# Kernel optimization log

Measured on AMD Instinct MI355X. Metric: run time of the kernel, lower is better.

## Reference

```python
import jax, jax.numpy as jnp
import numpy as np
from jax import lax

B, CH, TS = 64, 9, 3000
D, H, EMB = 64, 256, 32
WIDTHS = (3, 2, 2, 2, 2, 2)
IN_CH = (1, H, H, H, H, H)
OUT_CH = (H, H, H, H, H, D)


def setup_inputs():
    keys = iter(jax.random.split(jax.random.key(0), 64))
    inp = {"x": jax.random.normal(next(keys), (B, CH, TS), jnp.float32)}
    for l, (ci, co, w) in enumerate(zip(IN_CH, OUT_CH, WIDTHS)):
        inp[f"conv_w{l}"] = jax.random.normal(next(keys), (co, ci, w), jnp.float32) / np.float32(np.sqrt(ci * w))
        inp[f"conv_b{l}"] = jnp.zeros((co,), jnp.float32)
        inp[f"gn_g{l}"] = jnp.ones((co,), jnp.float32)
        inp[f"gn_b{l}"] = jnp.zeros((co,), jnp.float32)
    inp["ro_w"] = jax.random.normal(next(keys), (D, D), jnp.float32) / np.float32(np.sqrt(D))
    inp["ro_b"] = jnp.zeros((D,), jnp.float32)
    for r in range(2):
        inp[f"msg_w{r}"] = jax.random.normal(next(keys), (2 * D, D), jnp.float32) / np.float32(np.sqrt(2 * D))
        inp[f"msg_b{r}"] = jnp.zeros((D,), jnp.float32)
    inp["rn_w1"] = jax.random.normal(next(keys), (D, D), jnp.float32) / np.float32(np.sqrt(D))
    inp["rn_b1"] = jnp.zeros((D,), jnp.float32)
    inp["rn_w2"] = jax.random.normal(next(keys), (D, D), jnp.float32) / np.float32(np.sqrt(D))
    inp["rn_b2"] = jnp.zeros((D,), jnp.float32)
    inp["proj_w"] = jax.random.normal(next(keys), (D, EMB), jnp.float32) / np.float32(np.sqrt(D))
    inp["proj_b"] = jnp.zeros((EMB,), jnp.float32)
    return inp


def _gn(h, g, b):
    # GroupNorm(num_groups=1): normalize over (C, T) per sample
    mu = h.mean(axis=(1, 2), keepdims=True)
    var = h.var(axis=(1, 2), keepdims=True)
    return (h - mu) * lax.rsqrt(var + 1e-5) * g[None, :, None] + b[None, :, None]


def _forward(x, ps):
    b, ch, ts = x.shape
    h = x.reshape(b * ch, 1, ts)  # each view is one 1-channel node signal
    for l, w in enumerate(WIDTHS):
        W, bi, g, be = ps[4 * l], ps[4 * l + 1], ps[4 * l + 2], ps[4 * l + 3]
        h = lax.conv_general_dilated(h, W, (w,), [(w // 2, w // 2)], dimension_numbers=("NCH", "OIH", "NCH")) + bi[None, :, None]
        h = jax.nn.gelu(_gn(h, g, be), approximate=False)
    ro_w, ro_b = ps[24], ps[25]
    h = jnp.einsum("nct,co->not", h, ro_w) + ro_b[None, :, None]  # 1x1 readout conv
    lat = h.transpose(0, 2, 1)  # [b*ch, T, D]
    N = b * ch
    # fully-connected graph within each sample, exactly as in the torch code
    msg_from = np.repeat(np.arange(N), ch - 1)
    grid = np.broadcast_to(np.arange(N).reshape(b, ch)[:, None, :], (b, ch, ch))
    msg_to = grid[:, ~np.eye(ch, dtype=bool)].reshape(-1)
    for W, bi in ((ps[26], ps[27]), (ps[28], ps[29])):
        m = jnp.concatenate([lat[msg_from], lat[msg_to]], axis=-1)  # [E, T, 2D]
        m = jax.nn.relu(m @ W + bi) / (ch - 1)  # dropout is identity at eval
        lat = lat.at[msg_to].add(m)
    view_id = np.repeat(np.arange(b), ch)
    y = jax.ops.segment_sum(lat, view_id, num_segments=b)  # [b, T, D]
    y = (jax.nn.relu(y @ ps[30] + ps[31]) @ ps[32] + ps[33]) / ch
    return (y @ ps[34] + ps[35]).transpose(0, 2, 1)  # [b, EMB, T]


def reference(x, conv_w0, conv_b0, gn_g0, gn_b0, conv_w1, conv_b1, gn_g1, gn_b1, conv_w2, conv_b2, gn_g2, gn_b2, conv_w3, conv_b3, gn_g3, gn_b3, conv_w4, conv_b4, gn_g4, gn_b4, conv_w5, conv_b5, gn_g5, gn_b5, ro_w, ro_b, msg_w0, msg_b0, msg_w1, msg_b1, rn_w1, rn_b1, rn_w2, rn_b2, proj_w, proj_b):
    ps = (conv_w0, conv_b0, gn_g0, gn_b0, conv_w1, conv_b1, gn_g1, gn_b1, conv_w2, conv_b2, gn_g2, gn_b2, conv_w3, conv_b3, gn_g3, gn_b3, conv_w4, conv_b4, gn_g4, gn_b4, conv_w5, conv_b5, gn_g5, gn_b5, ro_w, ro_b, msg_w0, msg_b0, msg_w1, msg_b1, rn_w1, rn_b1, rn_w2, rn_b2, proj_w, proj_b)
    return _forward(x, ps)
```

## Files before the change

kernel.cpp:

```cpp
#include <hip/hip_runtime.h>
#include <hip/hip_bf16.h>

typedef __hip_bfloat16 bf16;
typedef __attribute__((ext_vector_type(8))) short s8v;
typedef __attribute__((ext_vector_type(4))) float f4v;

__device__ __forceinline__ float gelu_f(float x) {
    float x2 = x * x;
    float z  = x * __builtin_fmaf(0.071355f, x2, 1.595769f);
    float e  = __expf(-z);
    return x * __builtin_amdgcn_rcpf(1.0f + e);
}
__device__ __forceinline__ unsigned short f2bf_u(float f) {
    bf16 b = __float2bfloat16(f);
    return *(unsigned short*)&b;
}
__device__ __forceinline__ float bfu2f(unsigned short u) {
    bf16 b = *(bf16*)&u;
    return __bfloat162float(b);
}

__global__ __launch_bounds__(256) void zero_k(float* __restrict__ p, int n) {
    int i = blockIdx.x * 256 + threadIdx.x;
    if (i < n) p[i] = 0.f;
}

__global__ __launch_bounds__(256) void wcvt_k(
    const float* __restrict__ w1, const float* __restrict__ w2,
    const float* __restrict__ w3, const float* __restrict__ w4,
    const float* __restrict__ w5, bf16* __restrict__ dst)
{
    int i = blockIdx.x * 256 + threadIdx.x;
    if (i >= 557056) return;
    const float* src; int li;
    if      (i < 131072) { src = w1; li = i; }
    else if (i < 262144) { src = w2; li = i - 131072; }
    else if (i < 393216) { src = w3; li = i - 262144; }
    else if (i < 524288) { src = w4; li = i - 393216; }
    else                 { src = w5; li = i - 524288; }
    int co = li >> 9, rem = li & 511;
    int kc = rem >> 6, rr = rem & 63;
    int s = rr >> 5, cil = rr & 31;
    dst[i] = __float2bfloat16(src[co * 512 + (kc * 32 + cil) * 2 + s]);
}

__global__ __launch_bounds__(256) void m0red_k(
    const float* __restrict__ W0, const float* __restrict__ b0,
    float* __restrict__ coef, float* __restrict__ w0t)
{
    __shared__ float red[256];
    const int co = threadIdx.x;
    float w0 = W0[3 * co], w1 = W0[3 * co + 1], w2 = W0[3 * co + 2], b = b0[co];
    w0t[co] = w0; w0t[256 + co] = w1; w0t[512 + co] = w2;
    float vals[14] = {w0, w1, w2, b,
                      w0 * w0, w1 * w1, w2 * w2, b * b,
                      2.f * w0 * w1, 2.f * w0 * w2, 2.f * w1 * w2,
                      2.f * w0 * b, 2.f * w1 * b, 2.f * w2 * b};
    for (int k = 0; k < 14; k++) {
        red[co] = vals[k];
        __syncthreads();
        for (int st = 128; st > 0; st >>= 1) {
            if (co < st) red[co] += red[co + st];
            __syncthreads();
        }
        if (co == 0) coef[k] = red[0];
        __syncthreads();
    }
}

__global__ __launch_bounds__(256) void c0stats_k(
    const float* __restrict__ x, const float* __restrict__ coef,
    float* __restrict__ mu0, float* __restrict__ rstd0)
{
    __shared__ float xsl[3008];
    __shared__ float red[512];
    const int n = blockIdx.x, tid = threadIdx.x;
    const float* xr = x + (size_t)n * 3000;
    for (int i = tid; i < 750; i += 256) *(float4*)&xsl[4 + 4 * i] = *(const float4*)(xr + 4 * i);
    if (tid < 4) xsl[tid] = 0.f;
    float c[14];
    #pragma unroll
    for (int k = 0; k < 14; k++) c[k] = coef[k];
    __syncthreads();
    float S = 0.f, Q = 0.f;
    if (tid < 250) {
        float f[16];
        #pragma unroll
        for (int k = 0; k < 4; k++) *(float4*)&f[4 * k] = *(const float4*)&xsl[12 * tid + 4 * k];
        #pragma unroll
        for (int j = 0; j < 4; j++) {
            float x0 = f[3 * j + 3], x1 = f[3 * j + 4], x2 = f[3 * j + 5];
            S += c[0] * x0 + c[1] * x1 + c[2] * x2 + c[3];
            Q += c[4] * x0 * x0 + c[5] * x1 * x1 + c[6] * x2 * x2 + c[7]
               + c[8] * x0 * x1 + c[9] * x0 * x2 + c[10] * x1 * x2
               + c[11] * x0 + c[12] * x1 + c[13] * x2;
        }
    }
    red[tid] = S; red[256 + tid] = Q;
    __syncthreads();
    for (int st = 128; st > 0; st >>= 1) {
        if (tid < st) { red[tid] += red[tid + st]; red[256 + tid] += red[256 + tid + st]; }
        __syncthreads();
    }
    if (tid == 0) {
        float m = red[0] * (1.f / 256000.f);
        float var = red[256] * (1.f / 256000.f) - m * m;
        mu0[n] = m;
        rstd0[n] = rsqrtf(var + 1e-5f);
    }
}

template<int MW, int NW, int MODE>
__global__ __launch_bounds__(256) void convT_k(
    const bf16* __restrict__ g, const float* __restrict__ xraw,
    const float* __restrict__ w0t, const bf16* __restrict__ Wp,
    const float* __restrict__ bias, const float* __restrict__ b0c,
    bf16* __restrict__ hout, float* __restrict__ ssum, float* __restrict__ ssq,
    int T_g, int T_out, int n0,
    const float* __restrict__ pssum, const float* __restrict__ pssq,
    const float* __restrict__ pgam, const float* __restrict__ pbet,
    float pinvCT)
{
    constexpr int CO = 4 * NW * 16;
    constexpr int MT = MW * 16;
    constexpr int NSLOT = MT * 8;
    constexpr int NU = (NSLOT + 255) / 256;
    __shared__ bf16 aT[MT * 64];
    __shared__ float biasS[CO];
    __shared__ float red[512];
    __shared__ float acoS[256], ccoS[256];
    __shared__ float xs[(MODE == 2) ? 400 : 1];
    __shared__ float w0s[(MODE == 2) ? 768 : 1];
    const int n  = blockIdx.y;
    const int t0 = blockIdx.x * MT;
    const int tid = threadIdx.x;
    for (int i = tid; i < CO; i += 256) biasS[i] = bias[i];
    if (MODE == 1) {
        float mu = pssum[n0 + n] * pinvCT;
        float rs = rsqrtf(pssq[n0 + n] * pinvCT - mu * mu + 1e-5f);
        float a = rs * pgam[tid];
        acoS[tid] = a;
        ccoS[tid] = pbet[tid] - mu * a;
        __syncthreads();
    } else {
        float mu = pssum[n];
        float rs = pssq[n];
        float a = rs * pgam[tid];
        acoS[tid] = a;
        ccoS[tid] = (b0c[tid] - mu) * a + pbet[tid];
        for (int i = tid; i < 768; i += 256) w0s[i] = w0t[i];
        const float* xr = xraw + (size_t)n * 3000;
        for (int i = tid; i < 400; i += 256) {
            int xg = 6 * t0 - 4 + i;
            xs[i] = ((unsigned)xg < 3000u) ? xr[xg] : 0.f;
        }
        __syncthreads();
    }
    const int w = tid >> 6, lane = tid & 63;
    const int l16 = lane & 15, quad = lane >> 4;
    const int sx = l16 & 7;
    const bf16* gb = (MODE == 2) ? nullptr : (g + (size_t)n * T_g * 256);

    bool s_inv[NU];
    int s_q[NU], s_tin[NU], s_off[NU];
    #pragma unroll
    for (int u = 0; u < NU; u++) {
        int slot = tid + 256 * u;
        s_inv[u] = (NSLOT % 256 != 0) && (slot >= NSLOT);
        if (s_inv[u]) { s_tin[u] = 0x7fffffff; s_q[u] = 0; s_off[u] = 0; continue; }
        int t = slot >> 3, j = slot & 7;
        int ks = j >> 2, q = j & 3;
        s_q[u] = q;
        s_tin[u] = 2 * (t0 + t) - 1 + ks;
        s_off[u] = (t * 8 + (j ^ (t & 7))) * 8;
    }

    f4v acc[MW][NW];
    #pragma unroll
    for (int i = 0; i < MW; i++)
        #pragma unroll
        for (int j = 0; j < NW; j++) acc[i][j] = (f4v){0.f, 0.f, 0.f, 0.f};

    for (int kc = 0; kc < 8; kc++) {
        #pragma unroll
        for (int u = 0; u < NU; u++) {
            if (s_inv[u]) continue;
            int tin = s_tin[u];
            s8v v = (s8v){0, 0, 0, 0, 0, 0, 0, 0};
            if ((unsigned)tin < (unsigned)T_g) {
                const int ci0 = kc * 32 + s_q[u] * 8;
                float4 a0 = *(const float4*)&acoS[ci0], a1 = *(const float4*)&acoS[ci0 + 4];
                float4 c0 = *(const float4*)&ccoS[ci0], c1 = *(const float4*)&ccoS[ci0 + 4];
                float av[8] = {a0.x, a0.y, a0.z, a0.w, a1.x, a1.y, a1.z, a1.w};
                float cv[8] = {c0.x, c0.y, c0.z, c0.w, c1.x, c1.y, c1.z, c1.w};
                unsigned short* uu = (unsigned short*)&v;
                if (MODE == 2) {
                    int lx = 3 * (tin - 2 * t0) + 3;
                    float x0 = xs[lx], x1 = xs[lx + 1], x2 = xs[lx + 2];
                    float4 wa0 = *(const float4*)&w0s[ci0],       wa1 = *(const float4*)&w0s[ci0 + 4];
                    float4 wb0 = *(const float4*)&w0s[256 + ci0], wb1 = *(const float4*)&w0s[256 + ci0 + 4];
                    float4 wc0 = *(const float4*)&w0s[512 + ci0], wc1 = *(const float4*)&w0s[512 + ci0 + 4];
                    float wav[8] = {wa0.x, wa0.y, wa0.z, wa0.w, wa1.x, wa1.y, wa1.z, wa1.w};
                    float wbv[8] = {wb0.x, wb0.y, wb0.z, wb0.w, wb1.x, wb1.y, wb1.z, wb1.w};
                    float wcv[8] = {wc0.x, wc0.y, wc0.z, wc0.w, wc1.x, wc1.y, wc1.z, wc1.w};
                    #pragma unroll
                    for (int jj = 0; jj < 8; jj++) {
                        float conv = wav[jj] * x0 + wbv[jj] * x1 + wcv[jj] * x2;
                        uu[jj] = f2bf_u(gelu_f(conv * av[jj] + cv[jj]));
                    }
                } else {
                    v = *(const s8v*)(gb + (size_t)tin * 256 + ci0);
                    #pragma unroll
                    for (int jj = 0; jj < 8; jj++)
                        uu[jj] = f2bf_u(gelu_f(bfu2f(uu[jj]) * av[jj] + cv[jj]));
                }
            }
            *(s8v*)&aT[s_off[u]] = v;
        }
        s8v bfr[2][NW];
        #pragma unroll
        for (int ks = 0; ks < 2; ks++)
            #pragma unroll
            for (int j = 0; j < NW; j++) {
                int co = w * NW * 16 + j * 16 + l16;
                bfr[ks][j] = *(const s8v*)(Wp + (size_t)co * 512 + kc * 64 + ks * 32 + quad * 8);
            }
        __syncthreads();
        __builtin_amdgcn_s_setprio(1);
        #pragma unroll
        for (int ks = 0; ks < 2; ks++) {
            const int sl = (ks * 4 + quad) ^ sx;
            s8v af[MW];
            #pragma unroll
            for (int i = 0; i < MW; i++)
                af[i] = *(const s8v*)&aT[(i * 16 + l16) * 64 + sl * 8];
            #pragma unroll
            for (int i = 0; i < MW; i++)
                #pragma unroll
                for (int j = 0; j < NW; j++)
                    acc[i][j] = __builtin_amdgcn_mfma_f32_16x16x32_bf16(af[i], bfr[ks][j], acc[i][j], 0, 0, 0);
        }
        __builtin_amdgcn_s_setprio(0);
        __syncthreads();
    }

    float lsum = 0.f, lsq = 0.f;
    #pragma unroll
    for (int i = 0; i < MW; i++) {
        #pragma unroll
        for (int r = 0; r < 4; r++) {
            int t = t0 + i * 16 + quad * 4 + r;
            if (t < T_out) {
                bf16* orow = hout + ((size_t)n * T_out + t) * CO;
                #pragma unroll
                for (int j = 0; j < NW; j++) {
                    int co = w * NW * 16 + j * 16 + l16;
                    float v = acc[i][j][r] + biasS[co];
                    orow[co] = __float2bfloat16(v);
                    lsum += v; lsq += v * v;
                }
            }
        }
    }
    red[tid] = lsum; red[256 + tid] = lsq;
    __syncthreads();
    for (int st = 128; st > 0; st >>= 1) {
        if (tid < st) { red[tid] += red[tid + st]; red[256 + tid] += red[256 + tid + st]; }
        __syncthreads();
    }
    if (tid == 0) { atomicAdd(&ssum[n0 + n], red[0]); atomicAdd(&ssq[n0 + n], red[256]); }
}

__global__ __launch_bounds__(256) void readout_pre_k(
    const bf16* __restrict__ h5T, const float* __restrict__ row,
    const float* __restrict__ rob, const float* __restrict__ g5,
    const float* __restrict__ be5, const float* __restrict__ ssum,
    const float* __restrict__ ssq, float invCT,
    const float* __restrict__ mw, const float* __restrict__ mb,
    float* __restrict__ lat0, float* __restrict__ A0, float* __restrict__ Bv0)
{
    __shared__ float lh[2112];
    __shared__ float ll[2112];
    __shared__ float lw[8192];
    __shared__ float lb[64];
    const int n = blockIdx.x, tid = threadIdx.x;
    const float mu = ssum[n] * invCT;
    const float rs = rsqrtf(ssq[n] * invCT - mu * mu + 1e-5f);
    for (int idx = tid; idx < 2112; idx += 256) {
        int c = idx & 63;
        float a = rs * g5[c];
        float v = __bfloat162float(h5T[(size_t)n * 2112 + idx]) * a + (be5[c] - mu * a);
        lh[idx] = gelu_f(v);
    }
    for (int idx = tid; idx < 4096; idx += 256) lw[idx] = row[idx];
    if (tid < 64) lb[tid] = rob[tid];
    __syncthreads();
    for (int idx = tid; idx < 2112; idx += 256) {
        int t = idx >> 6, d = idx & 63;
        float a = lb[d];
        #pragma unroll 8
        for (int c = 0; c < 64; c++) a += lh[t * 64 + c] * lw[c * 64 + d];
        ll[idx] = a;
        lat0[(size_t)n * 2112 + idx] = a;
    }
    __syncthreads();
    for (int idx = tid; idx < 8192; idx += 256) lw[idx] = mw[idx];
    if (tid < 64) lb[tid] = mb[tid];
    __syncthreads();
    for (int idx = tid; idx < 2112; idx += 256) {
        int t = idx >> 6, d = idx & 63;
        float a = 0.f, bb = lb[d];
        #pragma unroll 8
        for (int k = 0; k < 64; k++) {
            float xv = ll[t * 64 + k];
            a  += xv * lw[k * 64 + d];
            bb += xv * lw[(64 + k) * 64 + d];
        }
        A0[(size_t)n * 2112 + idx]  = a;
        Bv0[(size_t)n * 2112 + idx] = bb;
    }
}

__global__ __launch_bounds__(256) void comb_pre_k(
    const float* __restrict__ lat0, const float* __restrict__ A0,
    const float* __restrict__ Bv0, const float* __restrict__ mw,
    const float* __restrict__ mb, float* __restrict__ lat1,
    float* __restrict__ A1, float* __restrict__ Bv1)
{
    __shared__ float ll[2112];
    __shared__ float lw[8192];
    __shared__ float lb[64];
    const int n = blockIdx.x, tid = threadIdx.x;
    const int b9 = (n / 9) * 9, j = n - b9;
    for (int idx = tid; idx < 2112; idx += 256) {
        float base = Bv0[(size_t)n * 2112 + idx];
        float s = 0.f;
        #pragma unroll
        for (int i = 0; i < 9; i++) {
            if (i == j) continue;
            s += fmaxf(A0[(size_t)(b9 + i) * 2112 + idx] + base, 0.f);
        }
        float v = lat0[(size_t)n * 2112 + idx] + s * 0.125f;
        ll[idx] = v;
        lat1[(size_t)n * 2112 + idx] = v;
    }
    for (int idx = tid; idx < 8192; idx += 256) lw[idx] = mw[idx];
    if (tid < 64) lb[tid] = mb[tid];
    __syncthreads();
    for (int idx = tid; idx < 2112; idx += 256) {
        int t = idx >> 6, d = idx & 63;
        float a = 0.f, bb = lb[d];
        #pragma unroll 8
        for (int k = 0; k < 64; k++) {
            float xv = ll[t * 64 + k];
            a  += xv * lw[k * 64 + d];
            bb += xv * lw[(64 + k) * 64 + d];
        }
        A1[(size_t)n * 2112 + idx]  = a;
        Bv1[(size_t)n * 2112 + idx] = bb;
    }
}

__global__ __launch_bounds__(256) void final2_k(
    const float* __restrict__ lat1, const float* __restrict__ A1,
    const float* __restrict__ Bv1,
    const float* __restrict__ w1, const float* __restrict__ b1,
    const float* __restrict__ w2, const float* __restrict__ b2,
    const float* __restrict__ pw, const float* __restrict__ pb,
    float* __restrict__ out)
{
    __shared__ float ly[2112], lz[2112];
    __shared__ float lw1[4096], lw2[4096], lpw[2048];
    __shared__ float lb1[64], lb2[64], lpb[32];
    const int b = blockIdx.x, tid = threadIdx.x;
    for (int idx = tid; idx < 4096; idx += 256) { lw1[idx] = w1[idx]; lw2[idx] = w2[idx]; }
    for (int idx = tid; idx < 2048; idx += 256) lpw[idx] = pw[idx];
    if (tid < 64) { lb1[tid] = b1[tid]; lb2[tid] = b2[tid]; }
    if (tid < 32) lpb[tid] = pb[tid];
    for (int idx = tid; idx < 2112; idx += 256) {
        float Av[9], Bb[9], s = 0.f;
        #pragma unroll
        for (int jj = 0; jj < 9; jj++) {
            size_t off = ((size_t)(b * 9 + jj)) * 2112 + idx;
            Av[jj] = A1[off];
            Bb[jj] = Bv1[off];
            s += lat1[off];
        }
        float m = 0.f;
        #pragma unroll
        for (int jj = 0; jj < 9; jj++) {
            float rowsum = 0.f;
            #pragma unroll
            for (int ii = 0; ii < 9; ii++) rowsum += fmaxf(Av[ii] + Bb[jj], 0.f);
            m += rowsum - fmaxf(Av[jj] + Bb[jj], 0.f);
        }
        ly[idx] = s + m * 0.125f;
    }
    __syncthreads();
    for (int idx = tid; idx < 2112; idx += 256) {
        int t = idx >> 6, d = idx & 63;
        float s = lb1[d];
        #pragma unroll 8
        for (int k = 0; k < 64; k++) s += ly[t * 64 + k] * lw1[k * 64 + d];
        lz[idx] = fmaxf(s, 0.f);
    }
    __syncthreads();
    for (int idx = tid; idx < 2112; idx += 256) {
        int t = idx >> 6, d = idx & 63;
        float s = lb2[d];
        #pragma unroll 8
        for (int k = 0; k < 64; k++) s += lz[t * 64 + k] * lw2[k * 64 + d];
        ly[idx] = s * (1.f / 9.f);
    }
    __syncthreads();
    for (int idx = tid; idx < 1056; idx += 256) {
        int e = idx / 33, t = idx - e * 33;
        float s = lpb[e];
        #pragma unroll 8
        for (int d = 0; d < 64; d++) s += ly[t * 64 + d] * lpw[d * 32 + e];
        out[(size_t)b * 1056 + idx] = s;
    }
}

extern "C" void kernel_launch(void* const* d_in, const int* in_sizes, int n_in,
                              void* d_out, int out_size, void* d_ws, size_t ws_size,
                              hipStream_t stream)
{
    const float* x = (const float*)d_in[0];
    const float* cw[6]; const float* cb[6]; const float* gg[6]; const float* gb[6];
    for (int l = 0; l < 6; l++) {
        cw[l] = (const float*)d_in[1 + 4 * l];
        cb[l] = (const float*)d_in[2 + 4 * l];
        gg[l] = (const float*)d_in[3 + 4 * l];
        gb[l] = (const float*)d_in[4 + 4 * l];
    }
    const float* ro_w = (const float*)d_in[25];
    const float* ro_b = (const float*)d_in[26];
    const float* mw0  = (const float*)d_in[27];
    const float* mb0  = (const float*)d_in[28];
    const float* mw1  = (const float*)d_in[29];
    const float* mb1  = (const float*)d_in[30];
    const float* rw1  = (const float*)d_in[31];
    const float* rb1  = (const float*)d_in[32];
    const float* rw2  = (const float*)d_in[33];
    const float* rb2  = (const float*)d_in[34];
    const float* pw   = (const float*)d_in[35];
    const float* pb   = (const float*)d_in[36];

    char* ws = (char*)d_ws;
    bf16* h1T  = (bf16*)(ws);
    bf16* h2T  = (bf16*)(ws + 147750912);
    bf16* h3T  = (bf16*)(ws + 221773824);
    bf16* h4T  = (bf16*)(ws);
    bf16* h5T  = (bf16*)(ws + 147750912);
    float* lat0 = (float*)(ws);
    float* A0   = lat0 + 1216512;
    float* Bv0  = A0   + 1216512;
    float* lat1 = Bv0  + 1216512;
    float* A1   = lat1 + 1216512;
    float* Bv1  = A1   + 1216512;
    float* stat  = (float*)(ws + 258932736);
    float* mu0   = stat;
    float* rstd0 = stat + 576;
    float* coef  = stat + 1152;
    float* ssumA = stat + 1168;
    float* ssqA  = ssumA + 5 * 576;
    float* w0taps = ssqA + 5 * 576;
    bf16*  Wp    = (bf16*)(ws + 258965504);
    #define SSUM(l) (ssumA + ((l) - 1) * 576)
    #define SSQ(l)  (ssqA  + ((l) - 1) * 576)

    zero_k<<<(5760 + 255) / 256, 256, 0, stream>>>(ssumA, 2 * 5 * 576);
    wcvt_k<<<(557056 + 255) / 256, 256, 0, stream>>>(cw[1], cw[2], cw[3], cw[4], cw[5], Wp);
    m0red_k<<<1, 256, 0, stream>>>(cw[0], cb[0], coef, w0taps);
    c0stats_k<<<576, 256, 0, stream>>>(x, coef, mu0, rstd0);

    convT_k<4, 4, 2><<<dim3(8, 576), 256, 0, stream>>>(
        nullptr, x, w0taps, Wp, cb[1], cb[0], h1T, SSUM(1), SSQ(1), 1000, 501, 0,
        mu0, rstd0, gg[0], gb[0], 0.f);

    convT_k<4, 4, 1><<<dim3(4, 576), 256, 0, stream>>>(
        h1T, nullptr, nullptr, Wp + 131072, cb[2], nullptr, h2T, SSUM(2), SSQ(2), 501, 251, 0,
        SSUM(1), SSQ(1), gg[1], gb[1], 1.f / (256.f * 501.f));

    convT_k<4, 4, 1><<<dim3(2, 576), 256, 0, stream>>>(
        h2T, nullptr, nullptr, Wp + 262144, cb[3], nullptr, h3T, SSUM(3), SSQ(3), 251, 126, 0,
        SSUM(2), SSQ(2), gg[2], gb[2], 1.f / (256.f * 251.f));

    convT_k<4, 4, 1><<<dim3(1, 576), 256, 0, stream>>>(
        h3T, nullptr, nullptr, Wp + 393216, cb[4], nullptr, h4T, SSUM(4), SSQ(4), 126, 64, 0,
        SSUM(3), SSQ(3), gg[3], gb[3], 1.f / (256.f * 126.f));

    convT_k<3, 1, 1><<<dim3(1, 576), 256, 0, stream>>>(
        h4T, nullptr, nullptr, Wp + 524288, cb[5], nullptr, h5T, SSUM(5), SSQ(5), 64, 33, 0,
        SSUM(4), SSQ(4), gg[4], gb[4], 1.f / (256.f * 64.f));

    readout_pre_k<<<576, 256, 0, stream>>>(h5T, ro_w, ro_b, gg[5], gb[5],
                                           SSUM(5), SSQ(5), 1.f / (64.f * 33.f),
                                           mw0, mb0, lat0, A0, Bv0);
    comb_pre_k<<<576, 256, 0, stream>>>(lat0, A0, Bv0, mw1, mb1, lat1, A1, Bv1);
    final2_k<<<64, 256, 0, stream>>>(lat1, A1, Bv1, rw1, rb1, rw2, rb2, pw, pb, (float*)d_out);
}
```

Measured before the change: 647.4 us.

## Stage full K tile in LDS upfront and halve time tile per block

Each conv block now covers 32 output time steps instead of 64. Each thread loads and normalizes its single slot for all 8 K-chunks into a larger shared buffer up front, then runs the MFMA loop with no per-chunk barriers. The grid doubles to give more blocks, and per-iteration syncs are removed so loads overlap better. The costs are more LDS per block (32KB for aT), which may reduce occupancy, and weight fragments are reloaded by twice as many blocks. The last layer also drops from 3 M-tiles to 2 across 2 blocks.

```diff
diff --git a/kernel.cpp b/kernel.cpp
--- a/kernel.cpp
+++ b/kernel.cpp
@@ -110,7 +110,7 @@
     }
 }
 
-template<int MW, int NW, int MODE>
+template<int NW, int MODE>
 __global__ __launch_bounds__(256) void convT_k(
     const bf16* __restrict__ g, const float* __restrict__ xraw,
     const float* __restrict__ w0t, const bf16* __restrict__ Wp,
@@ -122,14 +122,12 @@
     float pinvCT)
 {
     constexpr int CO = 4 * NW * 16;
-    constexpr int MT = MW * 16;
-    constexpr int NSLOT = MT * 8;
-    constexpr int NU = (NSLOT + 255) / 256;
-    __shared__ bf16 aT[MT * 64];
+    constexpr int MT = 32;
+    __shared__ bf16 aT[8 * 2048];
     __shared__ float biasS[CO];
     __shared__ float red[512];
     __shared__ float acoS[256], ccoS[256];
-    __shared__ float xs[(MODE == 2) ? 400 : 1];
+    __shared__ float xs[(MODE == 2) ? 200 : 1];
     __shared__ float w0s[(MODE == 2) ? 768 : 1];
     const int n  = blockIdx.y;
     const int t0 = blockIdx.x * MT;
@@ -141,7 +139,6 @@
         float a = rs * pgam[tid];
         acoS[tid] = a;
         ccoS[tid] = pbet[tid] - mu * a;
-        __syncthreads();
     } else {
         float mu = pssum[n];
         float rs = pssq[n];
@@ -150,73 +147,83 @@
         ccoS[tid] = (b0c[tid] - mu) * a + pbet[tid];
         for (int i = tid; i < 768; i += 256) w0s[i] = w0t[i];
         const float* xr = xraw + (size_t)n * 3000;
-        for (int i = tid; i < 400; i += 256) {
-            int xg = 6 * t0 - 4 + i;
-            xs[i] = ((unsigned)xg < 3000u) ? xr[xg] : 0.f;
-        }
-        __syncthreads();
-    }
+        if (tid < 200) {
+            int xg = 6 * t0 - 4 + tid;
+            xs[tid] = ((unsigned)xg < 3000u) ? xr[xg] : 0.f;
+        }
+    }
+    __syncthreads();
+
     const int w = tid >> 6, lane = tid & 63;
     const int l16 = lane & 15, quad = lane >> 4;
     const int sx = l16 & 7;
     const bf16* gb = (MODE == 2) ? nullptr : (g + (size_t)n * T_g * 256);
 
-    bool s_inv[NU];
-    int s_q[NU], s_tin[NU], s_off[NU];
-    #pragma unroll
-    for (int u = 0; u < NU; u++) {
-        int slot = tid + 256 * u;
-        s_inv[u] = (NSLOT % 256 != 0) && (slot >= NSLOT);
-        if (s_inv[u]) { s_tin[u] = 0x7fffffff; s_q[u] = 0; s_off[u] = 0; continue; }
-        int t = slot >> 3, j = slot & 7;
-        int ks = j >> 2, q = j & 3;
-        s_q[u] = q;
-        s_tin[u] = 2 * (t0 + t) - 1 + ks;
-        s_off[u] = (t * 8 + (j ^ (t & 7))) * 8;
-    }
-
-    f4v acc[MW][NW];
-    #pragma unroll
-    for (int i = 0; i < MW; i++)
-        #pragma unroll
-        for (int j = 0; j < NW; j++) acc[i][j] = (f4v){0.f, 0.f, 0.f, 0.f};
-
-    for (int kc = 0; kc < 8; kc++) {
-        #pragma unroll
-        for (int u = 0; u < NU; u++) {
-            if (s_inv[u]) continue;
-            int tin = s_tin[u];
+    const int st_ = tid >> 3, j_ = tid & 7;
+    const int ks_ = j_ >> 2, q_ = j_ & 3;
+    const int tin = 2 * (t0 + st_) - 1 + ks_;
+    const int soff = (st_ * 8 + (j_ ^ (st_ & 7))) * 8;
+    const bool inb = (unsigned)tin < (unsigned)T_g;
+
+    if (MODE == 2) {
+        float x0 = 0.f, x1 = 0.f, x2 = 0.f;
+        if (inb) {
+            int lx = 3 * (tin - 2 * t0) + 3;
+            x0 = xs[lx]; x1 = xs[lx + 1]; x2 = xs[lx + 2];
+        }
+        #pragma unroll
+        for (int kc = 0; kc < 8; kc++) {
             s8v v = (s8v){0, 0, 0, 0, 0, 0, 0, 0};
-            if ((unsigned)tin < (unsigned)T_g) {
-                const int ci0 = kc * 32 + s_q[u] * 8;
+            if (inb) {
+                const int ci0 = kc * 32 + q_ * 8;
+                float4 a0 = *(const float4*)&acoS[ci0], a1 = *(const float4*)&acoS[ci0 + 4];
+                float4 c0 = *(const float4*)&ccoS[ci0], c1 = *(const float4*)&ccoS[ci0 + 4];
+                float4 wa0 = *(const float4*)&w0s[ci0],       wa1 = *(const float4*)&w0s[ci0 + 4];
+                float4 wb0 = *(const float4*)&w0s[256 + ci0], wb1 = *(const float4*)&w0s[256 + ci0 + 4];
+                float4 wc0 = *(const float4*)&w0s[512 + ci0], wc1 = *(const float4*)&w0s[512 + ci0 + 4];
+                float av[8]  = {a0.x, a0.y, a0.z, a0.w, a1.x, a1.y, a1.z, a1.w};
+                float cv[8]  = {c0.x, c0.y, c0.z, c0.w, c1.x, c1.y, c1.z, c1.w};
+                float wav[8] = {wa0.x, wa0.y, wa0.z, wa0.w, wa1.x, wa1.y, wa1.z, wa1.w};
+                float wbv[8] = {wb0.x, wb0.y, wb0.z, wb0.w, wb1.x, wb1.y, wb1.z, wb1.w};
+                float wcv[8] = {wc0.x, wc0.y, wc0.z, wc0.w, wc1.x, wc1.y, wc1.z, wc1.w};
+                unsigned short* uu = (unsigned short*)&v;
+                #pragma unroll
+                for (int jj = 0; jj < 8; jj++) {
+                    float conv = wav[jj] * x0 + wbv[jj] * x1 + wcv[jj] * x2;
+                    uu[jj] = f2bf_u(gelu_f(__builtin_fmaf(conv, av[jj], cv[jj])));
+                }
+            }
+            *(s8v*)&aT[kc * 2048 + soff] = v;
+        }
+    } else {
+        #pragma unroll
+        for (int kc = 0; kc < 8; kc++) {
+            s8v v = (s8v){0, 0, 0, 0, 0, 0, 0, 0};
+            if (inb) {
+                const int ci0 = kc * 32 + q_ * 8;
                 float4 a0 = *(const float4*)&acoS[ci0], a1 = *(const float4*)&acoS[ci0 + 4];
                 float4 c0 = *(const float4*)&ccoS[ci0], c1 = *(const float4*)&ccoS[ci0 + 4];
                 float av[8] = {a0.x, a0.y, a0.z, a0.w, a1.x, a1.y, a1.z, a1.w};
                 float cv[8] = {c0.x, c0.y, c0.z, c0.w, c1.x, c1.y, c1.z, c1.w};
+                v = *(const s8v*)(gb + (size_t)tin * 256 + ci0);
                 unsigned short* uu = (unsigned short*)&v;
-                if (MODE == 2) {
-                    int lx = 3 * (tin - 2 * t0) + 3;
-                    float x0 = xs[lx], x1 = xs[lx + 1], x2 = xs[lx + 2];
-                    float4 wa0 = *(const float4*)&w0s[ci0],       wa1 = *(const float4*)&w0s[ci0 + 4];
-                    float4 wb0 = *(const float4*)&w0s[256 + ci0], wb1 = *(const float4*)&w0s[256 + ci0 + 4];
-                    float4 wc0 = *(const float4*)&w0s[512 + ci0], wc1 = *(const float4*)&w0s[512 + ci0 + 4];
-                    float wav[8] = {wa0.x, wa0.y, wa0.z, wa0.w, wa1.x, wa1.y, wa1.z, wa1.w};
-                    float wbv[8] = {wb0.x, wb0.y, wb0.z, wb0.w, wb1.x, wb1.y, wb1.z, wb1.w};
-                    float wcv[8] = {wc0.x, wc0.y, wc0.z, wc0.w, wc1.x, wc1.y, wc1.z, wc1.w};
-                    #pragma unroll
-                    for (int jj = 0; jj < 8; jj++) {
-                        float conv = wav[jj] * x0 + wbv[jj] * x1 + wcv[jj] * x2;
-                        uu[jj] = f2bf_u(gelu_f(conv * av[jj] + cv[jj]));
-                    }
-                } else {
-                    v = *(const s8v*)(gb + (size_t)tin * 256 + ci0);
-                    #pragma unroll
-                    for (int jj = 0; jj < 8; jj++)
-                        uu[jj] = f2bf_u(gelu_f(bfu2f(uu[jj]) * av[jj] + cv[jj]));
-                }
+                #pragma unroll
+                for (int jj = 0; jj < 8; jj++)
+                    uu[jj] = f2bf_u(gelu_f(__builtin_fmaf(bfu2f(uu[jj]), av[jj], cv[jj])));
             }
-            *(s8v*)&aT[s_off[u]] = v;
-        }
+            *(s8v*)&aT[kc * 2048 + soff] = v;
+        }
+    }
+    __syncthreads();
+
+    f4v acc[2][NW];
+    #pragma unroll
+    for (int i = 0; i < 2; i++)
+        #pragma unroll
+        for (int j = 0; j < NW; j++) acc[i][j] = (f4v){0.f, 0.f, 0.f, 0.f};
+
+    #pragma unroll
+    for (int kc = 0; kc < 8; kc++) {
         s8v bfr[2][NW];
         #pragma unroll
         for (int ks = 0; ks < 2; ks++)
@@ -225,28 +232,27 @@
                 int co = w * NW * 16 + j * 16 + l16;
                 bfr[ks][j] = *(const s8v*)(Wp + (size_t)co * 512 + kc * 64 + ks * 32 + quad * 8);
             }
-        __syncthreads();
+        const bf16* rb = aT + kc * 2048;
         __builtin_amdgcn_s_setprio(1);
         #pragma unroll
         for (int ks = 0; ks < 2; ks++) {
             const int sl = (ks * 4 + quad) ^ sx;
-            s8v af[MW];
+            s8v af[2];
             #pragma unroll
-            for (int i = 0; i < MW; i++)
-                af[i] = *(const s8v*)&aT[(i * 16 + l16) * 64 + sl * 8];
+            for (int i = 0; i < 2; i++)
+                af[i] = *(const s8v*)&rb[(i * 16 + l16) * 64 + sl * 8];
             #pragma unroll
-            for (int i = 0; i < MW; i++)
+            for (int i = 0; i < 2; i++)
                 #pragma unroll
                 for (int j = 0; j < NW; j++)
                     acc[i][j] = __builtin_amdgcn_mfma_f32_16x16x32_bf16(af[i], bfr[ks][j], acc[i][j], 0, 0, 0);
         }
         __builtin_amdgcn_s_setprio(0);
-        __syncthreads();
     }
 
     float lsum = 0.f, lsq = 0.f;
     #pragma unroll
-    for (int i = 0; i < MW; i++) {
+    for (int i = 0; i < 2; i++) {
         #pragma unroll
         for (int r = 0; r < 4; r++) {
             int t = t0 + i * 16 + quad * 4 + r;
@@ -475,23 +481,23 @@
     m0red_k<<<1, 256, 0, stream>>>(cw[0], cb[0], coef, w0taps);
     c0stats_k<<<576, 256, 0, stream>>>(x, coef, mu0, rstd0);
 
-    convT_k<4, 4, 2><<<dim3(8, 576), 256, 0, stream>>>(
+    convT_k<4, 2><<<dim3(16, 576), 256, 0, stream>>>(
         nullptr, x, w0taps, Wp, cb[1], cb[0], h1T, SSUM(1), SSQ(1), 1000, 501, 0,
         mu0, rstd0, gg[0], gb[0], 0.f);
 
-    convT_k<4, 4, 1><<<dim3(4, 576), 256, 0, stream>>>(
+    convT_k<4, 1><<<dim3(8, 576), 256, 0, stream>>>(
         h1T, nullptr, nullptr, Wp + 131072, cb[2], nullptr, h2T, SSUM(2), SSQ(2), 501, 251, 0,
         SSUM(1), SSQ(1), gg[1], gb[1], 1.f / (256.f * 501.f));
 
-    convT_k<4, 4, 1><<<dim3(2, 576), 256, 0, stream>>>(
+    convT_k<4, 1><<<dim3(4, 576), 256, 0, stream>>>(
         h2T, nullptr, nullptr, Wp + 262144, cb[3], nullptr, h3T, SSUM(3), SSQ(3), 251, 126, 0,
         SSUM(2), SSQ(2), gg[2], gb[2], 1.f / (256.f * 251.f));
 
-    convT_k<4, 4, 1><<<dim3(1, 576), 256, 0, stream>>>(
+    convT_k<4, 1><<<dim3(2, 576), 256, 0, stream>>>(
         h3T, nullptr, nullptr, Wp + 393216, cb[4], nullptr, h4T, SSUM(4), SSQ(4), 126, 64, 0,
         SSUM(3), SSQ(3), gg[3], gb[3], 1.f / (256.f * 126.f));
 
-    convT_k<3, 1, 1><<<dim3(1, 576), 256, 0, stream>>>(
+    convT_k<1, 1><<<dim3(2, 576), 256, 0, stream>>>(
         h4T, nullptr, nullptr, Wp + 524288, cb[5], nullptr, h5T, SSUM(5), SSQ(5), 64, 33, 0,
         SSUM(4), SSQ(4), gg[4], gb[4], 1.f / (256.f * 64.f));
 
```

After: 842.4 us. 1.3x slower.
